# Performance work log

Measured on AMD Instinct MI355X. Metric: run time of the kernel, lower is better.

The kernel has to match this reference:

```python
import jax, jax.numpy as jnp
import numpy as np

N_NODES = 100000
N_EDGES = 3200000
D_NODE = 5            # per-node feature dim
D_IN = 2 * D_NODE     # 10, MLP input dim
D_HID = D_IN * 5      # 50, HIDDEN_DIM_MULTIPLIER = 5


def setup_inputs() -> dict:
    key = jax.random.key(0)
    ks = jax.random.split(key, 8)
    x = jax.random.normal(ks[0], (N_NODES, D_NODE), dtype=jnp.float32)
    edge_index = jax.random.randint(ks[1], (2, N_EDGES), 0, N_NODES, dtype=jnp.int64)
    s1 = 1.0 / np.sqrt(D_IN)
    s2 = 1.0 / np.sqrt(D_HID)
    W1 = jax.random.uniform(ks[2], (D_IN, D_HID), jnp.float32, -s1, s1)
    b1 = jax.random.uniform(ks[3], (D_HID,), jnp.float32, -s1, s1)
    W2 = jax.random.uniform(ks[4], (D_HID, D_HID), jnp.float32, -s2, s2)
    b2 = jax.random.uniform(ks[5], (D_HID,), jnp.float32, -s2, s2)
    W3 = jax.random.uniform(ks[6], (D_HID, 1), jnp.float32, -s2, s2)
    b3 = jax.random.uniform(ks[7], (1,), jnp.float32, -s2, s2)
    return {"x": x, "edge_index": edge_index, "W1": W1, "b1": b1,
            "W2": W2, "b2": b2, "W3": W3, "b3": b3}


def reference(x, edge_index, W1, b1, W2, b2, W3, b3):
    # gather src/tgt node features and concat -> [E, 2*D_NODE]
    ef = jnp.concatenate([x[edge_index[0]], x[edge_index[1]]], axis=-1)
    h = jax.nn.relu(ef @ W1 + b1)
    h = jax.nn.relu(h @ W2 + b2)
    return jax.nn.sigmoid(h @ W3 + b3)  # [E, 1]
```

## Files before the change

kernel.cpp:

```cpp
#include <hip/hip_runtime.h>
#include <hip/hip_bf16.h>

typedef short bf16x8 __attribute__((ext_vector_type(8)));
typedef float f32x4  __attribute__((ext_vector_type(4)));
typedef float f32x16 __attribute__((ext_vector_type(16)));

union fragU { f32x4 f; bf16x8 b; uint4 q; uint u[4]; };

__device__ inline ushort f2bf(float f) {
    union { float f; uint u; } v; v.f = f;
    uint r = (v.u + 0x7FFFu + ((v.u >> 16) & 1u)) >> 16;
    return (ushort)r;
}
__device__ inline uint packbf(float a, float b) {
    return (uint)f2bf(a) | ((uint)f2bf(b) << 16);
}
__device__ inline uint cvtpk(float lo, float hi) {
    uint r;
    asm("v_cvt_pk_bf16_f32 %0, %1, %2" : "=v"(r) : "v"(lo), "v"(hi));
    return r;
}

__global__ __launch_bounds__(256) void pack_x_kernel(
    const float* __restrict__ x, uint4* __restrict__ xp, int N)
{
    int i = blockIdx.x * blockDim.x + threadIdx.x;
    if (i >= N) return;
    const float* r = x + (size_t)i * 5;
    uint4 o;
    o.x = packbf(r[0], r[1]);
    o.y = packbf(r[2], r[3]);
    o.z = packbf(r[4], 1.0f);
    o.w = 0u;
    xp[i] = o;
}

__global__ __launch_bounds__(64) void pack_w_kernel(
    const float* __restrict__ W1, const float* __restrict__ b1,
    const float* __restrict__ W2, const float* __restrict__ b2,
    const float* __restrict__ W3, uint4* __restrict__ tab)
{
    const int lane = threadIdx.x;
    const int col  = lane & 31;
    const int hi   = lane >> 5;

    union { ushort s[8]; uint4 q; } u;
    #pragma unroll
    for (int T = 0; T < 2; ++T) {
        #pragma unroll
        for (int d = 0; d < 8; ++d) {
            int k = 8 * hi + d;
            int j = 32 * T + col;
            float v = 0.f;
            if (j < 50) {
                if (k < 5)                 v = W1[k * 50 + j];
                else if (k == 5)           v = b1[j];
                else if (k >= 8 && k < 13) v = W1[(k - 3) * 50 + j];
            } else if (j == 50 && k == 5)  v = 1.0f;
            u.s[d] = f2bf(v);
        }
        tab[T * 64 + lane] = u.q;
    }
    #pragma unroll
    for (int T = 0; T < 2; ++T) {
        #pragma unroll
        for (int s = 0; s < 4; ++s) {
            #pragma unroll
            for (int d = 0; d < 8; ++d) {
                int kg = 16 * s + 8 * hi + d;
                int j  = 32 * T + col;
                float v = 0.f;
                if (j < 50) {
                    if (kg < 50)       v = W2[kg * 50 + j];
                    else if (kg == 50) v = b2[j];
                }
                u.s[d] = f2bf(v);
            }
            tab[(2 + T * 4 + s) * 64 + lane] = u.q;
        }
    }
    #pragma unroll
    for (int s = 0; s < 4; ++s) {
        #pragma unroll
        for (int d = 0; d < 8; ++d) {
            int kg = 16 * s + 8 * hi + d;
            float v = (col == 0 && kg < 50) ? W3[kg] : 0.f;
            u.s[d] = f2bf(v);
        }
        tab[(10 + s) * 64 + lane] = u.q;
    }
}

__global__ __launch_bounds__(256, 4) void edge_mlp_mfma13(
    const uint4* __restrict__ xp,
    const uint4* __restrict__ wtab,
    const int* __restrict__ ei,
    const float* __restrict__ b3,
    float* __restrict__ out, int E, int NT)
{
    const int tid  = threadIdx.x;
    const int w    = tid >> 6;
    const int lane = tid & 63;
    const int col  = lane & 31;
    const int hi   = lane >> 5;
    const int G    = gridDim.x;

    fragU w1f[2], w2f[8], w3a[4];
    #pragma unroll
    for (int i = 0; i < 2; ++i) w1f[i].q = wtab[i * 64 + lane];
    #pragma unroll
    for (int i = 0; i < 8; ++i) w2f[i].q = wtab[(2 + i) * 64 + lane];
    #pragma unroll
    for (int i = 0; i < 4; ++i) w3a[i].q = wtab[(10 + i) * 64 + lane];
    asm volatile("" :
        "+v"(w1f[0].f), "+v"(w1f[1].f),
        "+v"(w2f[0].f), "+v"(w2f[1].f), "+v"(w2f[2].f), "+v"(w2f[3].f),
        "+v"(w2f[4].f), "+v"(w2f[5].f), "+v"(w2f[6].f), "+v"(w2f[7].f),
        "+v"(w3a[0].f), "+v"(w3a[1].f), "+v"(w3a[2].f), "+v"(w3a[3].f));

    const float b3s = b3[0];

    auto LOAD_IDX = [&](int t_) -> int {
        int tc = (t_ < NT) ? t_ : (NT - 1);
        int e = tc * 128 + w * 32 + col;
        if (e >= E) e = 0;
        return ei[(size_t)hi * (size_t)E + (size_t)e];
    };

    const f32x16 z16 = {0.f,0.f,0.f,0.f, 0.f,0.f,0.f,0.f,
                        0.f,0.f,0.f,0.f, 0.f,0.f,0.f,0.f};

    auto INTERFACE = [&](const f32x16& c0, const f32x16& c1, fragU* bf) {
        uint word[2][8];
        #pragma unroll
        for (int k = 0; k < 8; ++k) {
            word[0][k] = cvtpk(fmaxf(c0[2*k], 0.f), fmaxf(c0[2*k+1], 0.f));
            word[1][k] = cvtpk(fmaxf(c1[2*k], 0.f), fmaxf(c1[2*k+1], 0.f));
        }
        #pragma unroll
        for (int s = 0; s < 4; ++s) {
            #pragma unroll
            for (int n = 0; n < 2; ++n) {
                const int mD = 2 * s, mS = 2 * s + 1;
                uint D = word[mD >> 2][2 * (mD & 3) + n];
                uint S = word[mS >> 2][2 * (mS & 3) + n];
                asm volatile("v_permlane32_swap_b32 %0, %1" : "+v"(D), "+v"(S));
                bf[s].u[n]     = D;
                bf[s].u[2 + n] = S;
            }
        }
    };

    int t = blockIdx.x;
    if (t >= NT) return;

    fragU f0; f0.q = xp[LOAD_IDX(t)];
    int idx1 = LOAD_IDX(t + G);

    for (; t < NT; t += G) {
        fragU f1; f1.q = xp[idx1];
        idx1 = LOAD_IDX(t + 2 * G);

        f32x16 c1_0 = __builtin_amdgcn_mfma_f32_32x32x16_bf16(w1f[0].b, f0.b, z16, 0, 0, 0);
        f32x16 c1_1 = __builtin_amdgcn_mfma_f32_32x32x16_bf16(w1f[1].b, f0.b, z16, 0, 0, 0);

        fragU bf[4];
        INTERFACE(c1_0, c1_1, bf);

        f32x16 c2_0 = z16, c2_1 = z16;
        #pragma unroll
        for (int s = 0; s < 4; ++s) {
            c2_0 = __builtin_amdgcn_mfma_f32_32x32x16_bf16(w2f[s].b,     bf[s].b, c2_0, 0, 0, 0);
            c2_1 = __builtin_amdgcn_mfma_f32_32x32x16_bf16(w2f[4 + s].b, bf[s].b, c2_1, 0, 0, 0);
        }

        fragU bf2[4];
        INTERFACE(c2_0, c2_1, bf2);

        f32x16 c3 = z16;
        #pragma unroll
        for (int s = 0; s < 4; ++s)
            c3 = __builtin_amdgcn_mfma_f32_32x32x16_bf16(w3a[s].b, bf2[s].b, c3, 0, 0, 0);

        if (hi == 0) {
            int e = t * 128 + w * 32 + col;
            if (e < E) {
                float ex = __expf(-(c3[0] + b3s));
                out[e] = __builtin_amdgcn_rcpf(1.f + ex);
            }
        }

        f0 = f1;
    }
}

extern "C" void kernel_launch(void* const* d_in, const int* in_sizes, int n_in,
                              void* d_out, int out_size, void* d_ws, size_t ws_size,
                              hipStream_t stream) {
    const float* x  = (const float*)d_in[0];
    const int*   ei = (const int*)d_in[1];
    const float* W1 = (const float*)d_in[2];
    const float* b1 = (const float*)d_in[3];
    const float* W2 = (const float*)d_in[4];
    const float* b2 = (const float*)d_in[5];
    const float* W3 = (const float*)d_in[6];
    const float* b3 = (const float*)d_in[7];
    float* out = (float*)d_out;

    int E = in_sizes[1] / 2;
    int N = in_sizes[0] / 5;

    uint4* wtab = (uint4*)d_ws;
    uint4* xp   = (uint4*)((char*)d_ws + 32768);

    pack_w_kernel<<<1, 64, 0, stream>>>(W1, b1, W2, b2, W3, wtab);
    pack_x_kernel<<<(N + 255) / 256, 256, 0, stream>>>(x, xp, N);

    int NT = (E + 127) / 128;
    int grid = NT < 2048 ? NT : 2048;
    edge_mlp_mfma13<<<grid, 256, 0, stream>>>(xp, wtab, ei, b3, out, E, NT);
}
```

Measured before the change: 65.81 us.

## Split edge MLP into gather-materialize pass and streaming MFMA pass

Adds a separate kernel that gathers packed source and target node features per edge into a contiguous workspace buffer. The MLP kernel then streams these coalesced per-edge fragments instead of doing dependent index-then-gather loads inside the compute loop. The aim is to decouple gather latency from the MFMA pipeline. The cost is an extra round trip of about 100 MB through HBM plus an extra launch, and the path only runs if the workspace is large enough.

Result: slower. 115.3 us (+75.2%).

```diff
diff --git a/kernel.cpp b/kernel.cpp
--- a/kernel.cpp
+++ b/kernel.cpp
@@ -91,7 +91,122 @@
     }
 }
 
-__global__ __launch_bounds__(256, 4) void edge_mlp_mfma13(
+__global__ __launch_bounds__(256) void build_ef_kernel(
+    const uint4* __restrict__ xp, const int* __restrict__ ei,
+    uint4* __restrict__ efp, int E)
+{
+    int e = blockIdx.x * blockDim.x + threadIdx.x;
+    if (e >= E) return;
+    int s = __builtin_nontemporal_load(&ei[e]);
+    int t = __builtin_nontemporal_load(&ei[E + e]);
+    uint4 qs = xp[s];
+    uint4 qt = xp[t];
+    efp[2 * (size_t)e]     = qs;
+    efp[2 * (size_t)e + 1] = qt;
+}
+
+__global__ __launch_bounds__(256, 3) void edge_mlp_stream(
+    const uint4* __restrict__ efp,
+    const uint4* __restrict__ wtab,
+    const float* __restrict__ b3,
+    float* __restrict__ out, int E, int NT)
+{
+    const int tid  = threadIdx.x;
+    const int w    = tid >> 6;
+    const int lane = tid & 63;
+    const int col  = lane & 31;
+    const int hi   = lane >> 5;
+    const int G    = gridDim.x;
+
+    fragU w1f[2], w2f[8], w3a[4];
+    #pragma unroll
+    for (int i = 0; i < 2; ++i) w1f[i].q = wtab[i * 64 + lane];
+    #pragma unroll
+    for (int i = 0; i < 8; ++i) w2f[i].q = wtab[(2 + i) * 64 + lane];
+    #pragma unroll
+    for (int i = 0; i < 4; ++i) w3a[i].q = wtab[(10 + i) * 64 + lane];
+    asm volatile("" :
+        "+v"(w1f[0].f), "+v"(w1f[1].f),
+        "+v"(w2f[0].f), "+v"(w2f[1].f), "+v"(w2f[2].f), "+v"(w2f[3].f),
+        "+v"(w2f[4].f), "+v"(w2f[5].f), "+v"(w2f[6].f), "+v"(w2f[7].f),
+        "+v"(w3a[0].f), "+v"(w3a[1].f), "+v"(w3a[2].f), "+v"(w3a[3].f));
+
+    const float b3s = b3[0];
+
+    const f32x16 z16 = {0.f,0.f,0.f,0.f, 0.f,0.f,0.f,0.f,
+                        0.f,0.f,0.f,0.f, 0.f,0.f,0.f,0.f};
+
+    auto LOADF = [&](int t_) -> fragU {
+        int tc = (t_ < NT) ? t_ : (NT - 1);
+        int e = tc * 128 + w * 32 + col;
+        if (e >= E) e = E - 1;
+        fragU a; a.q = efp[2 * (size_t)e + (size_t)hi];
+        return a;
+    };
+
+    auto INTERFACE = [&](const f32x16& c0, const f32x16& c1, fragU* bf) {
+        uint word[2][8];
+        #pragma unroll
+        for (int k = 0; k < 8; ++k) {
+            word[0][k] = cvtpk(fmaxf(c0[2*k], 0.f), fmaxf(c0[2*k+1], 0.f));
+            word[1][k] = cvtpk(fmaxf(c1[2*k], 0.f), fmaxf(c1[2*k+1], 0.f));
+        }
+        #pragma unroll
+        for (int s = 0; s < 4; ++s) {
+            #pragma unroll
+            for (int n = 0; n < 2; ++n) {
+                const int mD = 2 * s, mS = 2 * s + 1;
+                uint D = word[mD >> 2][2 * (mD & 3) + n];
+                uint S = word[mS >> 2][2 * (mS & 3) + n];
+                asm volatile("v_permlane32_swap_b32 %0, %1" : "+v"(D), "+v"(S));
+                bf[s].u[n]     = D;
+                bf[s].u[2 + n] = S;
+            }
+        }
+    };
+
+    int t = blockIdx.x;
+    if (t >= NT) return;
+
+    fragU f0 = LOADF(t);
+
+    for (; t < NT; t += G) {
+        fragU f1 = LOADF(t + G);
+
+        f32x16 c1_0 = __builtin_amdgcn_mfma_f32_32x32x16_bf16(w1f[0].b, f0.b, z16, 0, 0, 0);
+        f32x16 c1_1 = __builtin_amdgcn_mfma_f32_32x32x16_bf16(w1f[1].b, f0.b, z16, 0, 0, 0);
+
+        fragU bf[4];
+        INTERFACE(c1_0, c1_1, bf);
+
+        f32x16 c2_0 = z16, c2_1 = z16;
+        #pragma unroll
+        for (int s = 0; s < 4; ++s) {
+            c2_0 = __builtin_amdgcn_mfma_f32_32x32x16_bf16(w2f[s].b,     bf[s].b, c2_0, 0, 0, 0);
+            c2_1 = __builtin_amdgcn_mfma_f32_32x32x16_bf16(w2f[4 + s].b, bf[s].b, c2_1, 0, 0, 0);
+        }
+
+        fragU bf2[4];
+        INTERFACE(c2_0, c2_1, bf2);
+
+        f32x16 c3 = z16;
+        #pragma unroll
+        for (int s = 0; s < 4; ++s)
+            c3 = __builtin_amdgcn_mfma_f32_32x32x16_bf16(w3a[s].b, bf2[s].b, c3, 0, 0, 0);
+
+        if (hi == 0) {
+            int e = t * 128 + w * 32 + col;
+            if (e < E) {
+                float ex = __expf(-(c3[0] + b3s));
+                out[e] = __builtin_amdgcn_rcpf(1.f + ex);
+            }
+        }
+
+        f0 = f1;
+    }
+}
+
+__global__ __launch_bounds__(256, 4) void edge_mlp_fused(
     const uint4* __restrict__ xp,
     const uint4* __restrict__ wtab,
     const int* __restrict__ ei,
@@ -210,13 +325,24 @@
     int E = in_sizes[1] / 2;
     int N = in_sizes[0] / 5;
 
+    const size_t XP_OFF  = 32768;
+    const size_t EFP_OFF = (size_t)4 << 20;
+    const size_t needed  = EFP_OFF + (size_t)E * 32;
+
     uint4* wtab = (uint4*)d_ws;
-    uint4* xp   = (uint4*)((char*)d_ws + 32768);
+    uint4* xp   = (uint4*)((char*)d_ws + XP_OFF);
 
     pack_w_kernel<<<1, 64, 0, stream>>>(W1, b1, W2, b2, W3, wtab);
     pack_x_kernel<<<(N + 255) / 256, 256, 0, stream>>>(x, xp, N);
 
     int NT = (E + 127) / 128;
     int grid = NT < 2048 ? NT : 2048;
-    edge_mlp_mfma13<<<grid, 256, 0, stream>>>(xp, wtab, ei, b3, out, E, NT);
-}
+
+    if (ws_size >= needed) {
+        uint4* efp = (uint4*)((char*)d_ws + EFP_OFF);
+        build_ef_kernel<<<(E + 255) / 256, 256, 0, stream>>>(xp, ei, efp, E);
+        edge_mlp_stream<<<grid, 256, 0, stream>>>(efp, wtab, b3, out, E, NT);
+    } else {
+        edge_mlp_fused<<<grid, 256, 0, stream>>>(xp, wtab, ei, b3, out, E, NT);
+    }
+}
```
